# Kernel optimization log

Measured on AMD Instinct MI355X. Metric: run time of the kernel, lower is better.

The kernel has to match this reference:

```python
import jax, jax.numpy as jnp
import numpy as np

B, N, C = 4, 1024, 256
E = 65536
HID = 256  # LAYERS = [256, 256, 256]

def _linear_init(key, out_dim, in_dim):
    kw, kb = jax.random.split(key)
    s = 1.0 / np.sqrt(in_dim)
    W = jax.random.uniform(kw, (out_dim, in_dim), jnp.float32, -s, s)
    b = jax.random.uniform(kb, (out_dim,), jnp.float32, -s, s)
    return W, b

def setup_inputs() -> dict:
    key = jax.random.key(0)
    ks = jax.random.split(key, 5)
    pooled_features = jax.random.normal(ks[0], (B, N, C), jnp.float32)
    edge_index = jax.random.randint(ks[1], (2, E), 0, B * N)  # [src; dst]
    W1, b1 = _linear_init(ks[2], HID, 2 * C)
    W2, b2 = _linear_init(ks[3], HID, 2 * HID)
    W3, b3 = _linear_init(ks[4], HID, 2 * HID)
    return {"pooled_features": pooled_features, "edge_index": edge_index,
            "W1": W1, "b1": b1, "W2": W2, "b2": b2, "W3": W3, "b3": b3}

def _edge_conv(x, src, dst, num_nodes, W, b):
    # PyG EdgeConv: x_j = x[src], x_i = x[dst]; msg = relu(fc([x_j - x_i, x_i]));
    # aggr='max' scatters messages onto dst nodes.
    x_i = x[dst]                                   # [E, d]
    x_j = x[src]                                   # [E, d]
    msg = jnp.concatenate([x_j - x_i, x_i], axis=-1)  # [E, 2d]
    msg = jax.nn.relu(msg @ W.T + b)               # [E, out]
    out = jax.ops.segment_max(msg, dst, num_segments=num_nodes)
    # empty segments -> -inf; PyG fills with 0, and relu messages are >= 0
    return jnp.maximum(out, 0.0)

def reference(pooled_features, edge_index, W1, b1, W2, b2, W3, b3):
    b_, n_, c_ = pooled_features.shape
    num_nodes = b_ * n_
    x = pooled_features.reshape(num_nodes, c_)
    src, dst = edge_index[0], edge_index[1]
    feats = [x]
    for W, bb in ((W1, b1), (W2, b2), (W3, b3)):
        x = _edge_conv(x, src, dst, num_nodes, W, bb)
        feats.append(x)
    related_features = jnp.concatenate(feats, axis=-1)  # [num_nodes, 1024]
    return related_features
```

## Files before the change

kernel.cpp:

```cpp
#include <hip/hip_runtime.h>
#include <hip/hip_bf16.h>


#define NODES 4096
#define EDGES 65536
#define OSTR 1024

typedef __attribute__((ext_vector_type(8))) short bf16x8;
typedef __attribute__((ext_vector_type(4))) float f32x4;

__device__ __forceinline__ unsigned short f2bf(float f) {
    unsigned int x = __float_as_uint(f);
    return (unsigned short)((x + 0x7fff + ((x >> 16) & 1)) >> 16);
}

__global__ __launch_bounds__(256) void k_init(const float* __restrict__ x0,
                                              float* __restrict__ out) {
    int idx = blockIdx.x * 256 + threadIdx.x;
    int node = idx >> 8, c = idx & 255;
    out[node * OSTR + c] = x0[idx];
}

__global__ __launch_bounds__(256) void k_wprep(const float* __restrict__ W0,
                                               const float* __restrict__ W1,
                                               const float* __restrict__ W2,
                                               short* __restrict__ Wp) {
    int layer = blockIdx.x >> 9;
    int idx = (blockIdx.x & 511) * 256 + threadIdx.x;
    const float* W = layer == 0 ? W0 : (layer == 1 ? W1 : W2);
    int n = idx >> 8, c = idx & 255;
    float v;
    if (n < 256) v = W[n * 512 + c];
    else         v = W[(n - 256) * 512 + 256 + c] - W[(n - 256) * 512 + c];
    Wp[layer * 131072 + idx] = (short)f2bf(v);
}

__global__ __launch_bounds__(256) void k_zero(int* __restrict__ cnt) {
    cnt[blockIdx.x * 256 + threadIdx.x] = 0;
}
__global__ __launch_bounds__(256) void k_hist(const int* __restrict__ dst,
                                              int* __restrict__ cnt) {
    int e = blockIdx.x * 256 + threadIdx.x;
    atomicAdd(&cnt[dst[e]], 1);
}
__global__ __launch_bounds__(256) void k_scan(int* __restrict__ cnt,
                                              int* __restrict__ offsets) {
    __shared__ int part[256];
    int t = threadIdx.x, base = t * 16;
    int loc[16], s = 0;
#pragma unroll
    for (int j = 0; j < 16; ++j) { loc[j] = cnt[base + j]; s += loc[j]; }
    part[t] = s;
    __syncthreads();
    for (int d = 1; d < 256; d <<= 1) {
        int v = (t >= d) ? part[t - d] : 0;
        __syncthreads();
        part[t] += v;
        __syncthreads();
    }
    int run = part[t] - s;
#pragma unroll
    for (int j = 0; j < 16; ++j) { offsets[base + j] = run; run += loc[j]; cnt[base + j] = 0; }
    if (t == 255) offsets[4096] = run;
}
__global__ __launch_bounds__(256) void k_scatter(const int* __restrict__ src,
                                                 const int* __restrict__ dst,
                                                 const int* __restrict__ offsets,
                                                 int* __restrict__ cursor,
                                                 int* __restrict__ srcS) {
    int e = blockIdx.x * 256 + threadIdx.x;
    int d = dst[e];
    int p = offsets[d] + atomicAdd(&cursor[d], 1);
    srcS[p] = src[e];
}

__global__ __launch_bounds__(256) void k_gemm(const float* __restrict__ X,
                                              const short* __restrict__ Wp,
                                              const float* __restrict__ bias,
                                              float* __restrict__ UW) {
    __shared__ __align__(16) short Alds[32 * 264];

    const int t = threadIdx.x;
    const int m0 = blockIdx.x * 32;
    const int nhalf = blockIdx.y;

    {
        int r = t >> 3, ch = t & 7;
        const float4* xr4 = (const float4*)(X + (size_t)(m0 + r) * OSTR + ch * 32);
        short* arow = &Alds[r * 264 + ch * 32];
#pragma unroll
        for (int jj = 0; jj < 4; ++jj) {
            float4 a = xr4[2 * jj], b = xr4[2 * jj + 1];
            int4 pk;
            unsigned short* u = (unsigned short*)&pk;
            u[0] = f2bf(a.x); u[1] = f2bf(a.y); u[2] = f2bf(a.z); u[3] = f2bf(a.w);
            u[4] = f2bf(b.x); u[5] = f2bf(b.y); u[6] = f2bf(b.z); u[7] = f2bf(b.w);
            *(int4*)(arow + jj * 8) = pk;
        }
    }
    __syncthreads();

    const int wave = t >> 6, lane = t & 63;
    const int lm = lane & 15, kq = lane >> 4;
    const int nb = nhalf * 256 + wave * 64;

    f32x4 acc[2][4];
#pragma unroll
    for (int mt = 0; mt < 2; ++mt)
#pragma unroll
        for (int nt = 0; nt < 4; ++nt) acc[mt][nt] = (f32x4){0.f, 0.f, 0.f, 0.f};

    const short* a0p = &Alds[lm * 264 + kq * 8];
    const short* a1p = a0p + 16 * 264;
    const short* bp = Wp + (size_t)(nb + lm) * 256 + kq * 8;

#pragma unroll
    for (int ks = 0; ks < 8; ++ks) {
        const int ko = ks * 32;
        bf16x8 a0 = *(const bf16x8*)(a0p + ko);
        bf16x8 a1 = *(const bf16x8*)(a1p + ko);
        bf16x8 b0 = *(const bf16x8*)(bp + ko);
        bf16x8 b1 = *(const bf16x8*)(bp + 16 * 256 + ko);
        bf16x8 b2 = *(const bf16x8*)(bp + 32 * 256 + ko);
        bf16x8 b3 = *(const bf16x8*)(bp + 48 * 256 + ko);
        acc[0][0] = __builtin_amdgcn_mfma_f32_16x16x32_bf16(a0, b0, acc[0][0], 0, 0, 0);
        acc[0][1] = __builtin_amdgcn_mfma_f32_16x16x32_bf16(a0, b1, acc[0][1], 0, 0, 0);
        acc[0][2] = __builtin_amdgcn_mfma_f32_16x16x32_bf16(a0, b2, acc[0][2], 0, 0, 0);
        acc[0][3] = __builtin_amdgcn_mfma_f32_16x16x32_bf16(a0, b3, acc[0][3], 0, 0, 0);
        acc[1][0] = __builtin_amdgcn_mfma_f32_16x16x32_bf16(a1, b0, acc[1][0], 0, 0, 0);
        acc[1][1] = __builtin_amdgcn_mfma_f32_16x16x32_bf16(a1, b1, acc[1][1], 0, 0, 0);
        acc[1][2] = __builtin_amdgcn_mfma_f32_16x16x32_bf16(a1, b2, acc[1][2], 0, 0, 0);
        acc[1][3] = __builtin_amdgcn_mfma_f32_16x16x32_bf16(a1, b3, acc[1][3], 0, 0, 0);
    }

#pragma unroll
    for (int nt = 0; nt < 4; ++nt) {
        int ncol = nb + nt * 16 + lm;
        float bc = (nhalf == 1) ? bias[ncol - 256] : 0.0f;
#pragma unroll
        for (int mt = 0; mt < 2; ++mt) {
#pragma unroll
            for (int p = 0; p < 4; ++p) {
                int erow = mt * 16 + kq * 4 + p;
                UW[(size_t)(m0 + erow) * 512 + ncol] = acc[mt][nt][p] + bc;
            }
        }
    }
}

__global__ __launch_bounds__(64) void k_edge(const float* __restrict__ UW,
                                             const int* __restrict__ offsets,
                                             const int* __restrict__ srcS,
                                             float* __restrict__ out,
                                             int ooff) {
    const int i = blockIdx.x;
    const int l = threadIdx.x;
    const int beg = offsets[i], end = offsets[i + 1];

    const float NEG = -3.4e38f;
    float4 m = {NEG, NEG, NEG, NEG};
    int e = beg;
    for (; e + 4 <= end; e += 4) {
        int s0 = srcS[e], s1 = srcS[e + 1], s2 = srcS[e + 2], s3 = srcS[e + 3];
        float4 v0 = *(const float4*)(UW + (size_t)s0 * 512 + l * 4);
        float4 v1 = *(const float4*)(UW + (size_t)s1 * 512 + l * 4);
        float4 v2 = *(const float4*)(UW + (size_t)s2 * 512 + l * 4);
        float4 v3 = *(const float4*)(UW + (size_t)s3 * 512 + l * 4);
        m.x = fmaxf(fmaxf(fmaxf(m.x, v0.x), fmaxf(v1.x, v2.x)), v3.x);
        m.y = fmaxf(fmaxf(fmaxf(m.y, v0.y), fmaxf(v1.y, v2.y)), v3.y);
        m.z = fmaxf(fmaxf(fmaxf(m.z, v0.z), fmaxf(v1.z, v2.z)), v3.z);
        m.w = fmaxf(fmaxf(fmaxf(m.w, v0.w), fmaxf(v1.w, v2.w)), v3.w);
    }
    for (; e < end; ++e) {
        int s = srcS[e];
        float4 v = *(const float4*)(UW + (size_t)s * 512 + l * 4);
        m.x = fmaxf(m.x, v.x); m.y = fmaxf(m.y, v.y);
        m.z = fmaxf(m.z, v.z); m.w = fmaxf(m.w, v.w);
    }
    float4 w = *(const float4*)(UW + (size_t)i * 512 + 256 + l * 4);
    float4 r;
    r.x = fmaxf(m.x + w.x, 0.0f);
    r.y = fmaxf(m.y + w.y, 0.0f);
    r.z = fmaxf(m.z + w.z, 0.0f);
    r.w = fmaxf(m.w + w.w, 0.0f);
    *(float4*)(out + (size_t)i * OSTR + ooff + l * 4) = r;
}

extern "C" void kernel_launch(void* const* d_in, const int* in_sizes, int n_in,
                              void* d_out, int out_size, void* d_ws, size_t ws_size,
                              hipStream_t stream) {
    const float* x0 = (const float*)d_in[0];
    const int* ei = (const int*)d_in[1];
    const int* srcIdx = ei;
    const int* dstIdx = ei + EDGES;
    float* out = (float*)d_out;

    char* w = (char*)d_ws;
    float* UW = (float*)w;
    short* Wp = (short*)(w + 8388608);
    int* offsets = (int*)(w + 8388608 + 786432);
    int* cnt = (int*)(w + 8388608 + 786432 + 16512);
    int* srcS = (int*)(w + 8388608 + 786432 + 16512 + 16384);

    k_init<<<NODES, 256, 0, stream>>>(x0, out);
    k_wprep<<<3 * 512, 256, 0, stream>>>((const float*)d_in[2], (const float*)d_in[4],
                                         (const float*)d_in[6], Wp);
    k_zero<<<16, 256, 0, stream>>>(cnt);
    k_hist<<<EDGES / 256, 256, 0, stream>>>(dstIdx, cnt);
    k_scan<<<1, 256, 0, stream>>>(cnt, offsets);
    k_scatter<<<EDGES / 256, 256, 0, stream>>>(srcIdx, dstIdx, offsets, cnt, srcS);

    for (int l = 0; l < 3; ++l) {
        k_gemm<<<dim3(NODES / 32, 2), 256, 0, stream>>>(out + l * 256, Wp + l * 131072,
                                                        (const float*)d_in[3 + 2 * l], UW);
        k_edge<<<NODES, 64, 0, stream>>>(UW, offsets, srcS, out, (l + 1) * 256);
    }
}
```

Measured before the change: 153.8 us.

## Store gathered edge projections and next-layer activations in bf16, fuse setup kernels

The gathered half of the per-node projection (U) is now written in bf16, which halves the bytes the edge-max gather reads per edge. The self term W stays fp32. The edge kernel also writes a bf16 copy of its output, so the next GEMM loads bf16 directly instead of converting fp32 rows. The init, weight-prep and zero kernels are merged into one launch, and the edge kernel packs four nodes per 256-thread block. The cost is that the max is taken over bf16-rounded values, a small accuracy loss, and the writes of the extra bf16 buffer.

New measurement: 145.7 us. -5.3%, faster.

```diff
diff --git a/kernel.cpp b/kernel.cpp
--- a/kernel.cpp
+++ b/kernel.cpp
@@ -13,31 +13,39 @@
     unsigned int x = __float_as_uint(f);
     return (unsigned short)((x + 0x7fff + ((x >> 16) & 1)) >> 16);
 }
-
-__global__ __launch_bounds__(256) void k_init(const float* __restrict__ x0,
-                                              float* __restrict__ out) {
-    int idx = blockIdx.x * 256 + threadIdx.x;
-    int node = idx >> 8, c = idx & 255;
-    out[node * OSTR + c] = x0[idx];
-}
-
-__global__ __launch_bounds__(256) void k_wprep(const float* __restrict__ W0,
+__device__ __forceinline__ float bf2f(unsigned short u) {
+    return __uint_as_float(((unsigned int)u) << 16);
+}
+
+__global__ __launch_bounds__(256) void k_setup(const float* __restrict__ x0,
+                                               float* __restrict__ out,
+                                               unsigned short* __restrict__ xbuf,
+                                               const float* __restrict__ W0,
                                                const float* __restrict__ W1,
                                                const float* __restrict__ W2,
-                                               short* __restrict__ Wp) {
-    int layer = blockIdx.x >> 9;
-    int idx = (blockIdx.x & 511) * 256 + threadIdx.x;
-    const float* W = layer == 0 ? W0 : (layer == 1 ? W1 : W2);
-    int n = idx >> 8, c = idx & 255;
-    float v;
-    if (n < 256) v = W[n * 512 + c];
-    else         v = W[(n - 256) * 512 + 256 + c] - W[(n - 256) * 512 + c];
-    Wp[layer * 131072 + idx] = (short)f2bf(v);
-}
-
-__global__ __launch_bounds__(256) void k_zero(int* __restrict__ cnt) {
-    cnt[blockIdx.x * 256 + threadIdx.x] = 0;
-}
+                                               short* __restrict__ Wp,
+                                               int* __restrict__ cnt) {
+    int b = blockIdx.x, t = threadIdx.x;
+    if (b < NODES) {
+        int idx = b * 256 + t;
+        float v = x0[idx];
+        out[b * OSTR + (idx & 255)] = v;
+        xbuf[idx] = f2bf(v);
+    } else if (b < NODES + 1536) {
+        int b2 = b - NODES;
+        int layer = b2 >> 9;
+        int idx = (b2 & 511) * 256 + t;
+        const float* W = layer == 0 ? W0 : (layer == 1 ? W1 : W2);
+        int n = idx >> 8, c = idx & 255;
+        float v;
+        if (n < 256) v = W[n * 512 + c];
+        else         v = W[(n - 256) * 512 + 256 + c] - W[(n - 256) * 512 + c];
+        Wp[layer * 131072 + idx] = (short)f2bf(v);
+    } else {
+        cnt[(b - NODES - 1536) * 256 + t] = 0;
+    }
+}
+
 __global__ __launch_bounds__(256) void k_hist(const int* __restrict__ dst,
                                               int* __restrict__ cnt) {
     int e = blockIdx.x * 256 + threadIdx.x;
@@ -74,10 +82,11 @@
     srcS[p] = src[e];
 }
 
-__global__ __launch_bounds__(256) void k_gemm(const float* __restrict__ X,
+__global__ __launch_bounds__(256) void k_gemm(const unsigned short* __restrict__ xbuf,
                                               const short* __restrict__ Wp,
                                               const float* __restrict__ bias,
-                                              float* __restrict__ UW) {
+                                              unsigned short* __restrict__ UWu,
+                                              float* __restrict__ UWw) {
     __shared__ __align__(16) short Alds[32 * 264];
 
     const int t = threadIdx.x;
@@ -86,23 +95,20 @@
 
     {
         int r = t >> 3, ch = t & 7;
-        const float4* xr4 = (const float4*)(X + (size_t)(m0 + r) * OSTR + ch * 32);
-        short* arow = &Alds[r * 264 + ch * 32];
-#pragma unroll
-        for (int jj = 0; jj < 4; ++jj) {
-            float4 a = xr4[2 * jj], b = xr4[2 * jj + 1];
-            int4 pk;
-            unsigned short* u = (unsigned short*)&pk;
-            u[0] = f2bf(a.x); u[1] = f2bf(a.y); u[2] = f2bf(a.z); u[3] = f2bf(a.w);
-            u[4] = f2bf(b.x); u[5] = f2bf(b.y); u[6] = f2bf(b.z); u[7] = f2bf(b.w);
-            *(int4*)(arow + jj * 8) = pk;
+        const int4* ps = (const int4*)(xbuf + (size_t)(m0 + r) * 256);
+        short* arow = &Alds[r * 264];
+#pragma unroll
+        for (int j = 0; j < 4; ++j) {
+            int c = ch + 8 * j;
+            *(int4*)(arow + c * 8) = ps[c];
         }
     }
     __syncthreads();
 
     const int wave = t >> 6, lane = t & 63;
     const int lm = lane & 15, kq = lane >> 4;
-    const int nb = nhalf * 256 + wave * 64;
+    const int nbl = wave * 64;
+    const int nb = nhalf * 256 + nbl;
 
     f32x4 acc[2][4];
 #pragma unroll
@@ -135,55 +141,63 @@
 
 #pragma unroll
     for (int nt = 0; nt < 4; ++nt) {
-        int ncol = nb + nt * 16 + lm;
-        float bc = (nhalf == 1) ? bias[ncol - 256] : 0.0f;
+        int nc = nbl + nt * 16 + lm;
+        float bc = (nhalf == 1) ? bias[nc] : 0.0f;
 #pragma unroll
         for (int mt = 0; mt < 2; ++mt) {
 #pragma unroll
             for (int p = 0; p < 4; ++p) {
                 int erow = mt * 16 + kq * 4 + p;
-                UW[(size_t)(m0 + erow) * 512 + ncol] = acc[mt][nt][p] + bc;
+                float v = acc[mt][nt][p] + bc;
+                size_t off = (size_t)(m0 + erow) * 256 + nc;
+                if (nhalf == 0) UWu[off] = f2bf(v);
+                else            UWw[off] = v;
             }
         }
     }
 }
 
-__global__ __launch_bounds__(64) void k_edge(const float* __restrict__ UW,
-                                             const int* __restrict__ offsets,
-                                             const int* __restrict__ srcS,
-                                             float* __restrict__ out,
-                                             int ooff) {
-    const int i = blockIdx.x;
-    const int l = threadIdx.x;
+__global__ __launch_bounds__(256) void k_edge(const unsigned short* __restrict__ UWu,
+                                              const float* __restrict__ UWw,
+                                              const int* __restrict__ offsets,
+                                              const int* __restrict__ srcS,
+                                              float* __restrict__ out,
+                                              unsigned short* __restrict__ xbuf,
+                                              int ooff) {
+    const int i = blockIdx.x * 4 + (threadIdx.x >> 6);
+    const int l = threadIdx.x & 63;
     const int beg = offsets[i], end = offsets[i + 1];
 
     const float NEG = -3.4e38f;
-    float4 m = {NEG, NEG, NEG, NEG};
+    float m0 = NEG, m1 = NEG, m2 = NEG, m3 = NEG;
     int e = beg;
     for (; e + 4 <= end; e += 4) {
         int s0 = srcS[e], s1 = srcS[e + 1], s2 = srcS[e + 2], s3 = srcS[e + 3];
-        float4 v0 = *(const float4*)(UW + (size_t)s0 * 512 + l * 4);
-        float4 v1 = *(const float4*)(UW + (size_t)s1 * 512 + l * 4);
-        float4 v2 = *(const float4*)(UW + (size_t)s2 * 512 + l * 4);
-        float4 v3 = *(const float4*)(UW + (size_t)s3 * 512 + l * 4);
-        m.x = fmaxf(fmaxf(fmaxf(m.x, v0.x), fmaxf(v1.x, v2.x)), v3.x);
-        m.y = fmaxf(fmaxf(fmaxf(m.y, v0.y), fmaxf(v1.y, v2.y)), v3.y);
-        m.z = fmaxf(fmaxf(fmaxf(m.z, v0.z), fmaxf(v1.z, v2.z)), v3.z);
-        m.w = fmaxf(fmaxf(fmaxf(m.w, v0.w), fmaxf(v1.w, v2.w)), v3.w);
+        ushort4 v0 = *(const ushort4*)(UWu + (size_t)s0 * 256 + l * 4);
+        ushort4 v1 = *(const ushort4*)(UWu + (size_t)s1 * 256 + l * 4);
+        ushort4 v2 = *(const ushort4*)(UWu + (size_t)s2 * 256 + l * 4);
+        ushort4 v3 = *(const ushort4*)(UWu + (size_t)s3 * 256 + l * 4);
+        m0 = fmaxf(fmaxf(fmaxf(m0, bf2f(v0.x)), fmaxf(bf2f(v1.x), bf2f(v2.x))), bf2f(v3.x));
+        m1 = fmaxf(fmaxf(fmaxf(m1, bf2f(v0.y)), fmaxf(bf2f(v1.y), bf2f(v2.y))), bf2f(v3.y));
+        m2 = fmaxf(fmaxf(fmaxf(m2, bf2f(v0.z)), fmaxf(bf2f(v1.z), bf2f(v2.z))), bf2f(v3.z));
+        m3 = fmaxf(fmaxf(fmaxf(m3, bf2f(v0.w)), fmaxf(bf2f(v1.w), bf2f(v2.w))), bf2f(v3.w));
     }
     for (; e < end; ++e) {
         int s = srcS[e];
-        float4 v = *(const float4*)(UW + (size_t)s * 512 + l * 4);
-        m.x = fmaxf(m.x, v.x); m.y = fmaxf(m.y, v.y);
-        m.z = fmaxf(m.z, v.z); m.w = fmaxf(m.w, v.w);
-    }
-    float4 w = *(const float4*)(UW + (size_t)i * 512 + 256 + l * 4);
+        ushort4 v = *(const ushort4*)(UWu + (size_t)s * 256 + l * 4);
+        m0 = fmaxf(m0, bf2f(v.x)); m1 = fmaxf(m1, bf2f(v.y));
+        m2 = fmaxf(m2, bf2f(v.z)); m3 = fmaxf(m3, bf2f(v.w));
+    }
+    float4 w = *(const float4*)(UWw + (size_t)i * 256 + l * 4);
     float4 r;
-    r.x = fmaxf(m.x + w.x, 0.0f);
-    r.y = fmaxf(m.y + w.y, 0.0f);
-    r.z = fmaxf(m.z + w.z, 0.0f);
-    r.w = fmaxf(m.w + w.w, 0.0f);
+    r.x = fmaxf(m0 + w.x, 0.0f);
+    r.y = fmaxf(m1 + w.y, 0.0f);
+    r.z = fmaxf(m2 + w.z, 0.0f);
+    r.w = fmaxf(m3 + w.w, 0.0f);
     *(float4*)(out + (size_t)i * OSTR + ooff + l * 4) = r;
+    ushort4 rb;
+    rb.x = f2bf(r.x); rb.y = f2bf(r.y); rb.z = f2bf(r.z); rb.w = f2bf(r.w);
+    *(ushort4*)(xbuf + (size_t)i * 256 + l * 4) = rb;
 }
 
 extern "C" void kernel_launch(void* const* d_in, const int* in_sizes, int n_in,
@@ -196,23 +210,26 @@
     float* out = (float*)d_out;
 
     char* w = (char*)d_ws;
-    float* UW = (float*)w;
+    unsigned short* UWu = (unsigned short*)w;
+    float* UWw = (float*)(w + 2097152);
+    unsigned short* xbuf = (unsigned short*)(w + 6291456);
     short* Wp = (short*)(w + 8388608);
-    int* offsets = (int*)(w + 8388608 + 786432);
-    int* cnt = (int*)(w + 8388608 + 786432 + 16512);
-    int* srcS = (int*)(w + 8388608 + 786432 + 16512 + 16384);
-
-    k_init<<<NODES, 256, 0, stream>>>(x0, out);
-    k_wprep<<<3 * 512, 256, 0, stream>>>((const float*)d_in[2], (const float*)d_in[4],
-                                         (const float*)d_in[6], Wp);
-    k_zero<<<16, 256, 0, stream>>>(cnt);
+    int* offsets = (int*)(w + 9175040);
+    int* cnt = (int*)(w + 9191552);
+    int* srcS = (int*)(w + 9207936);
+
+    k_setup<<<NODES + 1536 + 16, 256, 0, stream>>>(x0, out, xbuf,
+                                                   (const float*)d_in[2], (const float*)d_in[4],
+                                                   (const float*)d_in[6], Wp, cnt);
     k_hist<<<EDGES / 256, 256, 0, stream>>>(dstIdx, cnt);
     k_scan<<<1, 256, 0, stream>>>(cnt, offsets);
     k_scatter<<<EDGES / 256, 256, 0, stream>>>(srcIdx, dstIdx, offsets, cnt, srcS);
 
     for (int l = 0; l < 3; ++l) {
-        k_gemm<<<dim3(NODES / 32, 2), 256, 0, stream>>>(out + l * 256, Wp + l * 131072,
-                                                        (const float*)d_in[3 + 2 * l], UW);
-        k_edge<<<NODES, 64, 0, stream>>>(UW, offsets, srcS, out, (l + 1) * 256);
-    }
-}
+        k_gemm<<<dim3(NODES / 32, 2), 256, 0, stream>>>(xbuf, Wp + l * 131072,
+                                                        (const float*)d_in[3 + 2 * l],
+                                                        UWu, UWw);
+        k_edge<<<NODES / 4, 256, 0, stream>>>(UWu, UWw, offsets, srcS, out, xbuf,
+                                              (l + 1) * 256);
+    }
+}
```
